# Kernel tuning notes

Hardware: AMD Instinct MI355X
Metric: run time of the kernel (lower is better)

Reference implementation:

```python
import jax, jax.numpy as jnp
import numpy as np

NMS_THRESHOLD = 0.4
TOP_K = 1000
MAX_BOXES = 300
N_ANCHORS = 300000
N_CLASSES = 80
DET_DIM = 85


def setup_inputs() -> dict:
    key = jax.random.key(0)
    k1, k2, k3, k4 = jax.random.split(key, 4)
    # valid [y1, x1, y2, x2] boxes: top-left corner + positive height/width
    yx = jax.random.uniform(k1, (1, N_ANCHORS, 2), jnp.float32) * 512.0
    hw = jax.random.uniform(k2, (1, N_ANCHORS, 2), jnp.float32) * 64.0 + 1.0
    boxes = jnp.concatenate([yx, yx + hw], axis=-1)
    classification = jax.random.uniform(k3, (1, N_ANCHORS, N_CLASSES), jnp.float32)
    detections = jax.random.normal(k4, (1, N_ANCHORS, DET_DIM), jnp.float32)
    return {"boxes": boxes, "classification": classification, "detections": detections}


def _iou_matrix(b):
    # b: [K, 4] as [y1, x1, y2, x2]
    y1, x1, y2, x2 = b[:, 0], b[:, 1], b[:, 2], b[:, 3]
    area = (y2 - y1) * (x2 - x1)
    ih = jnp.clip(jnp.minimum(y2[:, None], y2[None, :]) - jnp.maximum(y1[:, None], y1[None, :]), 0.0)
    iw = jnp.clip(jnp.minimum(x2[:, None], x2[None, :]) - jnp.maximum(x1[:, None], x1[None, :]), 0.0)
    inter = ih * iw
    return inter / (area[:, None] + area[None, :] - inter + 1e-8)


def _nms_forward(boxes, classification, detections):
    b = boxes[0]                      # [N, 4]
    cls = classification[0]           # [N, C]
    det = detections[0]               # [N, D]
    scores = jnp.max(cls, axis=1)     # [N]
    # pre-NMS top-k filter (lax.top_k returns scores sorted descending)
    _, idx = jax.lax.top_k(scores, TOP_K)
    b_k = b[idx]                      # [K, 4]
    det_k = det[idx]                  # [K, D]
    iou = _iou_matrix(b_k)            # [K, K]
    # greedy NMS over score-sorted candidates: keep box i iff no higher-scoring
    # kept box overlaps it above the threshold
    def step(keep, i):
        suppressed = jnp.any(keep & (iou[i] > NMS_THRESHOLD))
        return keep.at[i].set(~suppressed), None
    keep, _ = jax.lax.scan(step, jnp.zeros(TOP_K, dtype=bool), jnp.arange(TOP_K))
    # first MAX_BOXES kept candidates (in score order), zero-padded
    pos = jnp.where(keep, jnp.arange(TOP_K), TOP_K)
    pos = jnp.sort(pos)[:MAX_BOXES]
    valid = pos < TOP_K
    sel = det_k[jnp.minimum(pos, TOP_K - 1)]          # [MAX_BOXES, D]
    out = jnp.where(valid[:, None], sel, 0.0)
    return out[None]                   # [1, MAX_BOXES, D]


def reference(boxes, classification, detections):
    return _nms_forward(boxes, classification, detections)
```

## Files before the change

### kernel.cpp

```cpp
#include <hip/hip_runtime.h>
#include <stdint.h>

typedef unsigned long long u64;

#define N_ANCH   300000
#define N_CLS    80
#define DET_DIM  85
#define TOPK     1000
#define MAXB     300
#define NMS_THR  0.4f
#define CAP      4096
#define NBH      32
#define N4       (N_ANCH / 4)
#define ITH      ((N4 + NBH*1024 - 1) / (NBH*1024))

#define OFF_SBITS   0
#define OFF_HA      300032
#define OFF_HB      304128
#define OFF_META    308224
#define OFF_CAND    308288
#define OFF_TOPK    316480
#define OFF_BOXK    317480
#define OFF_MASK    321480
#define OFF_KEEPL   353480

__device__ __forceinline__ uint32_t ld_b32(const uint32_t* p) {
    return __hip_atomic_load(p, __ATOMIC_RELAXED, __HIP_MEMORY_SCOPE_AGENT);
}
__device__ __forceinline__ u64 ld_b64(const u64* p) {
    return __hip_atomic_load(p, __ATOMIC_RELAXED, __HIP_MEMORY_SCOPE_AGENT);
}
__device__ __forceinline__ void st_b32(uint32_t* p, uint32_t v) {
    __hip_atomic_store(p, v, __ATOMIC_RELAXED, __HIP_MEMORY_SCOPE_AGENT);
}
__device__ __forceinline__ void st_b64(u64* p, u64 v) {
    __hip_atomic_store(p, v, __ATOMIC_RELAXED, __HIP_MEMORY_SCOPE_AGENT);
}
__device__ __forceinline__ void st_f4(float4* p, float4 v) {
    union { float4 f; u64 u[2]; } cv; cv.f = v;
    u64* q = (u64*)p;
    st_b64(q, cv.u[0]); st_b64(q + 1, cv.u[1]);
}
__device__ __forceinline__ float4 ld_f4(const float4* p) {
    union { float4 f; u64 u[2]; } cv;
    const u64* q = (const u64*)p;
    cv.u[0] = ld_b64(q); cv.u[1] = ld_b64(q + 1);
    return cv.f;
}

__device__ __forceinline__ void gb_arrive(uint32_t* bar) {
    __syncthreads();
    if (threadIdx.x == 0)
        __hip_atomic_fetch_add(bar, 1u, __ATOMIC_RELAXED, __HIP_MEMORY_SCOPE_AGENT);
}
__device__ __forceinline__ void gb_wait(uint32_t* bar, uint32_t target) {
    if (threadIdx.x == 0) {
        while (__hip_atomic_load(bar, __ATOMIC_RELAXED, __HIP_MEMORY_SCOPE_AGENT) < target)
            __builtin_amdgcn_s_sleep(1);
    }
    __syncthreads();
}

__global__ __launch_bounds__(256) void k_scores(const float4* __restrict__ cls4,
                                                uint32_t* __restrict__ sbits,
                                                uint32_t* __restrict__ ha,
                                                uint32_t* __restrict__ hb,
                                                uint32_t* __restrict__ meta) {
    int tid = threadIdx.x;
    if (blockIdx.x == 0) {
        if (tid == 0) { meta[4] = 0; meta[8] = 0; }
        for (int i = tid; i < 4096; i += 256) { ha[i] = 0; hb[i] = 0; }
    }
    int wave = tid >> 6, lane = tid & 63, g = lane >> 2, q = lane & 3;
    int row = blockIdx.x * 64 + wave * 16 + g;
    if (row >= N_ANCH) return;
    const float4* rp = cls4 + (size_t)row * 20;
    float m = -1.0f;
    #pragma unroll
    for (int k = 0; k < 5; k++) {
        float4 v = rp[q + k * 4];
        m = fmaxf(m, fmaxf(fmaxf(v.x, v.y), fmaxf(v.z, v.w)));
    }
    m = fmaxf(m, __shfl_xor(m, 1));
    m = fmaxf(m, __shfl_xor(m, 2));
    if (q == 0) sbits[row] = __float_as_uint(m);
}

__device__ __forceinline__ void agg_add(uint32_t* h, uint32_t bin, bool valid) {
    int lane = threadIdx.x & 63;
    bool done = !valid;
    while (true) {
        unsigned long long rem = __ballot(!done);
        if (rem == 0ull) break;
        int leader = __ffsll((long long)rem) - 1;
        uint32_t lbin = __shfl(bin, leader);
        bool mine = (!done) && (bin == lbin);
        unsigned long long grp = __ballot(mine);
        if (lane == leader) atomicAdd(&h[lbin], (uint32_t)__popcll(grp));
        done = done || mine;
    }
}

__device__ __forceinline__ void findthr_core(const uint32_t c[4], uint32_t* wred,
                                             uint32_t K, uint32_t* res) {
    int tid = threadIdx.x, lane = tid & 63, wave = tid >> 6;
    uint32_t s = c[0] + c[1] + c[2] + c[3];
    uint32_t x = s;
    #pragma unroll
    for (int off = 1; off < 64; off <<= 1) {
        uint32_t v = __shfl_up(x, off);
        if (lane >= off) x += v;
    }
    if (lane == 63) wred[wave] = x;
    __syncthreads();
    if (wave == 0) {
        uint32_t w = (lane < 16) ? wred[lane] : 0u;
        #pragma unroll
        for (int off = 1; off < 16; off <<= 1) {
            uint32_t v = __shfl_up(w, off);
            if (lane >= off) w += v;
        }
        if (lane < 16) wred[lane] = w;
    }
    __syncthreads();
    uint32_t base = (wave == 0) ? 0u : wred[wave - 1];
    uint32_t incl = base + x, excl = incl - s;
    if (excl < K && incl >= K) {
        uint32_t run = excl;
        #pragma unroll
        for (int k = 0; k < 4; k++) {
            uint32_t nr = run + c[k];
            if (run < K && nr >= K) { res[0] = 4095 - (tid * 4 + k); res[1] = run; }
            run = nr;
        }
    }
    __syncthreads();
}

#define MSW(i, w) ((i) * 16 + (((w) + (i)) & 15))

__global__ __launch_bounds__(1024) void k_select(const uint4* __restrict__ sb4,
                                                 uint32_t* __restrict__ ha,
                                                 uint32_t* __restrict__ hb,
                                                 uint32_t* __restrict__ meta,
                                                 u64* __restrict__ cand,
                                                 uint32_t* __restrict__ topk,
                                                 const float4* __restrict__ boxes4,
                                                 float4* __restrict__ boxk,
                                                 u64* __restrict__ M,
                                                 uint32_t* __restrict__ keepl,
                                                 const float* __restrict__ det,
                                                 float* __restrict__ out) {
    __shared__ __align__(16) u64 big[16000];
    __shared__ uint32_t wred[16];
    __shared__ uint32_t mr[2];
    __shared__ uint32_t kidS[MAXB];

    const int tid = threadIdx.x, wave = tid >> 6, lane = tid & 63;
    const int blk = blockIdx.x;
    uint32_t* bar = &meta[8];
    uint32_t* h = (uint32_t*)big;

    for (int i = tid; i < 4096; i += 1024) h[i] = 0;
    __syncthreads();
    for (int it = 0; it < ITH; it++) {
        int t4 = (it * NBH + blk) * 1024 + tid;
        bool v = t4 < N4;
        uint4 sv = v ? sb4[t4] : make_uint4(0, 0, 0, 0);
        agg_add(h, sv.x >> 20, v);
        agg_add(h, sv.y >> 20, v);
        agg_add(h, sv.z >> 20, v);
        agg_add(h, sv.w >> 20, v);
    }
    __syncthreads();
    for (int i = tid; i < 4096; i += 1024) { uint32_t v = h[i]; if (v) atomicAdd(&ha[i], v); }
    gb_arrive(bar); gb_wait(bar, NBH * 1);

    uint32_t c[4];
    {
        uint32_t* base = ha + 4u * (1023u - (uint32_t)tid);
        c[0] = ld_b32(base + 3); c[1] = ld_b32(base + 2);
        c[2] = ld_b32(base + 1); c[3] = ld_b32(base + 0);
    }
    findthr_core(c, wred, TOPK, mr);
    const uint32_t binA = mr[0], GA = mr[1];
    for (int i = tid; i < 4096; i += 1024) h[i] = 0;
    __syncthreads();
    for (int it = 0; it < ITH; it++) {
        int t4 = (it * NBH + blk) * 1024 + tid;
        if (t4 < N4) {
            uint4 sv = sb4[t4];
            if ((sv.x >> 20) == binA) atomicAdd(&h[(sv.x >> 8) & 0xFFFu], 1u);
            if ((sv.y >> 20) == binA) atomicAdd(&h[(sv.y >> 8) & 0xFFFu], 1u);
            if ((sv.z >> 20) == binA) atomicAdd(&h[(sv.z >> 8) & 0xFFFu], 1u);
            if ((sv.w >> 20) == binA) atomicAdd(&h[(sv.w >> 8) & 0xFFFu], 1u);
        }
    }
    __syncthreads();
    for (int i = tid; i < 4096; i += 1024) { uint32_t v = h[i]; if (v) atomicAdd(&hb[i], v); }
    gb_arrive(bar); gb_wait(bar, NBH * 2);

    {
        uint32_t* base = hb + 4u * (1023u - (uint32_t)tid);
        c[0] = ld_b32(base + 3); c[1] = ld_b32(base + 2);
        c[2] = ld_b32(base + 1); c[3] = ld_b32(base + 0);
    }
    findthr_core(c, wred, TOPK - GA, mr);
    const uint32_t T24 = (binA << 12) | mr[0];
    for (int it = 0; it < ITH; it++) {
        int t4 = (it * NBH + blk) * 1024 + tid;
        bool v = t4 < N4;
        uint4 sv = v ? sb4[t4] : make_uint4(0, 0, 0, 0);
        uint32_t sl[4] = {sv.x, sv.y, sv.z, sv.w};
        #pragma unroll
        for (int s = 0; s < 4; s++) {
            uint32_t sb = sl[s];
            bool m = v && ((sb >> 8) >= T24);
            unsigned long long b = __ballot(m);
            if (b) {
                int leader = __ffsll((long long)b) - 1;
                uint32_t base2 = 0;
                if (lane == leader) base2 = atomicAdd(&meta[4], (uint32_t)__popcll(b));
                base2 = __shfl(base2, leader);
                if (m) {
                    uint32_t p = base2 + (uint32_t)__popcll(b & ((1ull << lane) - 1ull));
                    uint32_t idx = (uint32_t)(t4 * 4 + s);
                    if (p < CAP) st_b64(&cand[p], ((u64)sb << 32) | (uint32_t)(~idx));
                }
            }
        }
    }
    gb_arrive(bar); gb_wait(bar, NBH * 3);

    u64* candS = big;
    uint32_t C = ld_b32(&meta[4]); if (C > CAP) C = CAP;
    uint32_t Cpad = (C + 63u) & ~63u;
    for (uint32_t t = tid; t < Cpad; t += 1024) candS[t] = (t < C) ? ld_b64(&cand[t]) : 0ull;
    __syncthreads();
    for (uint32_t i = (uint32_t)(blk * 16 + wave); i < C; i += NBH * 16) {
        u64 my = candS[i];
        uint32_t r = 0;
        for (uint32_t j0 = 0; j0 < Cpad; j0 += 64)
            r += (uint32_t)__popcll(__ballot(candS[j0 + lane] > my));
        if (r < TOPK && lane == 0) {
            uint32_t idx = ~(uint32_t)(my & 0xFFFFFFFFull);
            if (idx < N_ANCH) { st_b32(&topk[r], idx); st_f4(&boxk[r], boxes4[idx]); }
        }
    }
    gb_arrive(bar); gb_wait(bar, NBH * 4);

    float4* bks  = (float4*)big;
    float* areaS = (float*)((char*)big + 16000);
    for (int i = tid; i < TOPK; i += 1024) {
        float4 b = ld_f4(&boxk[i]);
        bks[i] = b;
        {
            #pragma clang fp contract(off)
            areaS[i] = (b.z - b.x) * (b.w - b.y);
        }
    }
    __syncthreads();
    for (int gw = blk * 16 + wave; gw < TOPK * 16; gw += NBH * 16) {
        int i = gw >> 4, w = gw & 15;
        int j = w * 64 + lane, jc = j < TOPK ? j : 0;
        float4 bi = bks[i], bj = bks[jc];
        bool ok;
        {
            #pragma clang fp contract(off)
            float ih = fminf(bi.z, bj.z) - fmaxf(bi.x, bj.x); ih = fmaxf(ih, 0.0f);
            float iw = fminf(bi.w, bj.w) - fmaxf(bi.y, bj.y); iw = fmaxf(iw, 0.0f);
            float inter = ih * iw;
            float denom = (areaS[i] + areaS[jc] - inter) + 1e-8f;
            ok = (j < TOPK) && (inter / denom > NMS_THR);
        }
        unsigned long long m = __ballot(ok);
        if (lane == 0) st_b64(&M[i * 16 + w], m);
    }
    gb_arrive(bar);

    if (blk == 0) {
        gb_wait(bar, NBH * 5);
        u64* MS = big;
        for (int t = tid; t < TOPK * 16; t += 1024) {
            int i = t >> 4, w = t & 15;
            MS[MSW(i, w)] = ld_b64(&M[t]);
        }
        __syncthreads();
        if (tid < 64) {
            u64 keptArr[16];
            #pragma unroll
            for (int cc = 0; cc < 16; cc++) {
                int i = cc * 64 + lane;
                u64 pre = 0ull, Mic = 0ull;
                if (i < TOPK) {
                    #pragma unroll
                    for (int w = 0; w < cc; w++) pre |= MS[MSW(i, w)] & keptArr[w];
                    Mic = MS[MSW(i, cc)];
                }
                unsigned long long pre_mask = __ballot(pre != 0ull);
                u64 kc = 0ull;
                const int lim = (cc == 15) ? (TOPK - 960) : 64;
                for (int k = 0; k < lim; k++) {
                    unsigned long long b = __ballot(((Mic >> k) & 1ull) != 0ull);
                    bool sup = (((pre_mask >> k) & 1ull) != 0ull) || ((b & kc) != 0ull);
                    kc |= sup ? 0ull : (1ull << k);
                }
                keptArr[cc] = kc;
            }
            uint32_t pfxw[16];
            uint32_t run = 0;
            #pragma unroll
            for (int w = 0; w < 16; w++) { pfxw[w] = run; run += (uint32_t)__popcll(keptArr[w]); }
            int total = (int)run; if (total > MAXB) total = MAXB;
            for (int r = total + lane; r < MAXB; r += 64) st_b32(&keepl[r], 0xFFFFFFFFu);
            #pragma unroll
            for (int w = 0; w < 16; w++) {
                int i = w * 64 + lane;
                if (i < TOPK) {
                    u64 kw = keptArr[w];
                    if ((kw >> lane) & 1ull) {
                        uint32_t rank = pfxw[w] + (uint32_t)__popcll(kw & ((1ull << lane) - 1ull));
                        if (rank < MAXB) st_b32(&keepl[rank], ld_b32(&topk[i]));
                    }
                }
            }
        }
    }
    gb_arrive(bar); gb_wait(bar, NBH * 6);

    if (tid < MAXB) kidS[tid] = ld_b32(&keepl[tid]);
    __syncthreads();
    int t = blk * 1024 + tid;
    if (t < MAXB * DET_DIM) {
        int r = t / DET_DIM, col = t - r * DET_DIM;
        uint32_t src = kidS[r];
        float v = 0.0f;
        if (src < N_ANCH) v = det[(size_t)src * DET_DIM + col];
        out[t] = v;
    }
}

extern "C" void kernel_launch(void* const* d_in, const int* in_sizes, int n_in,
                              void* d_out, int out_size, void* d_ws, size_t ws_size,
                              hipStream_t stream) {
    const float4* boxes4 = (const float4*)d_in[0];
    const float4* cls4   = (const float4*)d_in[1];
    const float*  det    = (const float*)d_in[2];
    float* out = (float*)d_out;
    uint32_t* ws = (uint32_t*)d_ws;

    uint32_t* sbits = ws + OFF_SBITS;
    uint32_t* ha    = ws + OFF_HA;
    uint32_t* hb    = ws + OFF_HB;
    uint32_t* meta  = ws + OFF_META;
    u64*      cand  = (u64*)(ws + OFF_CAND);
    uint32_t* topk  = ws + OFF_TOPK;
    float4*   boxk  = (float4*)(ws + OFF_BOXK);
    u64*      M     = (u64*)(ws + OFF_MASK);
    uint32_t* keepl = ws + OFF_KEEPL;

    k_scores<<<(N_ANCH + 63) / 64, 256, 0, stream>>>(cls4, sbits, ha, hb, meta);
    k_select<<<NBH, 1024, 0, stream>>>((const uint4*)sbits, ha, hb, meta, cand, topk,
                                       boxes4, boxk, M, keepl, det, out);
}
```

Measured before the change: 273.7 us.

## Split persistent select kernel into separate launches replacing software grid barriers

Replaces the single 32-block persistent kernel, which used atomic-counter grid barriers between phases, with six separate kernel launches. Each launch gets its own grid size: 80 blocks for the histograms and compaction, 96 for ranking, 250 for mask building, and 1 for the greedy scan. This is meant to remove barrier spin-wait cost and raise parallelism in each phase. The trade-off is added launch overhead and extra global-memory round trips between phases.

```diff
diff --git a/kernel.cpp b/kernel.cpp
--- a/kernel.cpp
+++ b/kernel.cpp
@@ -10,9 +10,11 @@
 #define MAXB     300
 #define NMS_THR  0.4f
 #define CAP      4096
-#define NBH      32
 #define N4       (N_ANCH / 4)
-#define ITH      ((N4 + NBH*1024 - 1) / (NBH*1024))
+
+#define NB_HIST  80
+#define NB_RANK  96
+#define NB_MASK  250
 
 #define OFF_SBITS   0
 #define OFF_HA      300032
@@ -22,44 +24,6 @@
 #define OFF_TOPK    316480
 #define OFF_BOXK    317480
 #define OFF_MASK    321480
-#define OFF_KEEPL   353480
-
-__device__ __forceinline__ uint32_t ld_b32(const uint32_t* p) {
-    return __hip_atomic_load(p, __ATOMIC_RELAXED, __HIP_MEMORY_SCOPE_AGENT);
-}
-__device__ __forceinline__ u64 ld_b64(const u64* p) {
-    return __hip_atomic_load(p, __ATOMIC_RELAXED, __HIP_MEMORY_SCOPE_AGENT);
-}
-__device__ __forceinline__ void st_b32(uint32_t* p, uint32_t v) {
-    __hip_atomic_store(p, v, __ATOMIC_RELAXED, __HIP_MEMORY_SCOPE_AGENT);
-}
-__device__ __forceinline__ void st_b64(u64* p, u64 v) {
-    __hip_atomic_store(p, v, __ATOMIC_RELAXED, __HIP_MEMORY_SCOPE_AGENT);
-}
-__device__ __forceinline__ void st_f4(float4* p, float4 v) {
-    union { float4 f; u64 u[2]; } cv; cv.f = v;
-    u64* q = (u64*)p;
-    st_b64(q, cv.u[0]); st_b64(q + 1, cv.u[1]);
-}
-__device__ __forceinline__ float4 ld_f4(const float4* p) {
-    union { float4 f; u64 u[2]; } cv;
-    const u64* q = (const u64*)p;
-    cv.u[0] = ld_b64(q); cv.u[1] = ld_b64(q + 1);
-    return cv.f;
-}
-
-__device__ __forceinline__ void gb_arrive(uint32_t* bar) {
-    __syncthreads();
-    if (threadIdx.x == 0)
-        __hip_atomic_fetch_add(bar, 1u, __ATOMIC_RELAXED, __HIP_MEMORY_SCOPE_AGENT);
-}
-__device__ __forceinline__ void gb_wait(uint32_t* bar, uint32_t target) {
-    if (threadIdx.x == 0) {
-        while (__hip_atomic_load(bar, __ATOMIC_RELAXED, __HIP_MEMORY_SCOPE_AGENT) < target)
-            __builtin_amdgcn_s_sleep(1);
-    }
-    __syncthreads();
-}
 
 __global__ __launch_bounds__(256) void k_scores(const float4* __restrict__ cls4,
                                                 uint32_t* __restrict__ sbits,
@@ -68,7 +32,7 @@
                                                 uint32_t* __restrict__ meta) {
     int tid = threadIdx.x;
     if (blockIdx.x == 0) {
-        if (tid == 0) { meta[4] = 0; meta[8] = 0; }
+        if (tid == 0) meta[4] = 0;
         for (int i = tid; i < 4096; i += 256) { ha[i] = 0; hb[i] = 0; }
     }
     int wave = tid >> 6, lane = tid & 63, g = lane >> 2, q = lane & 3;
@@ -137,122 +101,121 @@
     __syncthreads();
 }
 
-#define MSW(i, w) ((i) * 16 + (((w) + (i)) & 15))
-
-__global__ __launch_bounds__(1024) void k_select(const uint4* __restrict__ sb4,
-                                                 uint32_t* __restrict__ ha,
-                                                 uint32_t* __restrict__ hb,
-                                                 uint32_t* __restrict__ meta,
-                                                 u64* __restrict__ cand,
-                                                 uint32_t* __restrict__ topk,
-                                                 const float4* __restrict__ boxes4,
-                                                 float4* __restrict__ boxk,
-                                                 u64* __restrict__ M,
-                                                 uint32_t* __restrict__ keepl,
-                                                 const float* __restrict__ det,
-                                                 float* __restrict__ out) {
-    __shared__ __align__(16) u64 big[16000];
+__device__ __forceinline__ void load_bins(const uint32_t* __restrict__ hist, uint32_t c[4]) {
+    uint4 q = ((const uint4*)hist)[1023 - threadIdx.x];
+    c[0] = q.w; c[1] = q.z; c[2] = q.y; c[3] = q.x;
+}
+
+__global__ __launch_bounds__(1024) void k_histA(const uint4* __restrict__ sb4,
+                                                uint32_t* __restrict__ ha) {
+    __shared__ uint32_t h[4096];
+    int tid = threadIdx.x;
+    for (int i = tid; i < 4096; i += 1024) h[i] = 0;
+    __syncthreads();
+    int t4 = blockIdx.x * 1024 + tid;
+    bool v = t4 < N4;
+    uint4 sv = v ? sb4[t4] : make_uint4(0, 0, 0, 0);
+    agg_add(h, sv.x >> 20, v);
+    agg_add(h, sv.y >> 20, v);
+    agg_add(h, sv.z >> 20, v);
+    agg_add(h, sv.w >> 20, v);
+    __syncthreads();
+    for (int i = tid; i < 4096; i += 1024) { uint32_t c = h[i]; if (c) atomicAdd(&ha[i], c); }
+}
+
+__global__ __launch_bounds__(1024) void k_histB(const uint4* __restrict__ sb4,
+                                                const uint32_t* __restrict__ ha,
+                                                uint32_t* __restrict__ hb) {
+    __shared__ uint32_t h[4096];
     __shared__ uint32_t wred[16];
     __shared__ uint32_t mr[2];
-    __shared__ uint32_t kidS[MAXB];
-
-    const int tid = threadIdx.x, wave = tid >> 6, lane = tid & 63;
-    const int blk = blockIdx.x;
-    uint32_t* bar = &meta[8];
-    uint32_t* h = (uint32_t*)big;
-
+    int tid = threadIdx.x;
+    uint32_t c[4];
+    load_bins(ha, c);
+    findthr_core(c, wred, TOPK, mr);
+    uint32_t binA = mr[0];
     for (int i = tid; i < 4096; i += 1024) h[i] = 0;
     __syncthreads();
-    for (int it = 0; it < ITH; it++) {
-        int t4 = (it * NBH + blk) * 1024 + tid;
-        bool v = t4 < N4;
-        uint4 sv = v ? sb4[t4] : make_uint4(0, 0, 0, 0);
-        agg_add(h, sv.x >> 20, v);
-        agg_add(h, sv.y >> 20, v);
-        agg_add(h, sv.z >> 20, v);
-        agg_add(h, sv.w >> 20, v);
-    }
-    __syncthreads();
-    for (int i = tid; i < 4096; i += 1024) { uint32_t v = h[i]; if (v) atomicAdd(&ha[i], v); }
-    gb_arrive(bar); gb_wait(bar, NBH * 1);
-
+    int t4 = blockIdx.x * 1024 + tid;
+    if (t4 < N4) {
+        uint4 sv = sb4[t4];
+        if ((sv.x >> 20) == binA) atomicAdd(&h[(sv.x >> 8) & 0xFFFu], 1u);
+        if ((sv.y >> 20) == binA) atomicAdd(&h[(sv.y >> 8) & 0xFFFu], 1u);
+        if ((sv.z >> 20) == binA) atomicAdd(&h[(sv.z >> 8) & 0xFFFu], 1u);
+        if ((sv.w >> 20) == binA) atomicAdd(&h[(sv.w >> 8) & 0xFFFu], 1u);
+    }
+    __syncthreads();
+    for (int i = tid; i < 4096; i += 1024) { uint32_t v = h[i]; if (v) atomicAdd(&hb[i], v); }
+}
+
+__global__ __launch_bounds__(1024) void k_compact(const uint4* __restrict__ sb4,
+                                                  const uint32_t* __restrict__ ha,
+                                                  const uint32_t* __restrict__ hb,
+                                                  uint32_t* __restrict__ meta,
+                                                  u64* __restrict__ cand) {
+    __shared__ uint32_t wred[16];
+    __shared__ uint32_t mr[2];
+    int tid = threadIdx.x, lane = tid & 63;
     uint32_t c[4];
-    {
-        uint32_t* base = ha + 4u * (1023u - (uint32_t)tid);
-        c[0] = ld_b32(base + 3); c[1] = ld_b32(base + 2);
-        c[2] = ld_b32(base + 1); c[3] = ld_b32(base + 0);
-    }
+    load_bins(ha, c);
     findthr_core(c, wred, TOPK, mr);
-    const uint32_t binA = mr[0], GA = mr[1];
-    for (int i = tid; i < 4096; i += 1024) h[i] = 0;
-    __syncthreads();
-    for (int it = 0; it < ITH; it++) {
-        int t4 = (it * NBH + blk) * 1024 + tid;
-        if (t4 < N4) {
-            uint4 sv = sb4[t4];
-            if ((sv.x >> 20) == binA) atomicAdd(&h[(sv.x >> 8) & 0xFFFu], 1u);
-            if ((sv.y >> 20) == binA) atomicAdd(&h[(sv.y >> 8) & 0xFFFu], 1u);
-            if ((sv.z >> 20) == binA) atomicAdd(&h[(sv.z >> 8) & 0xFFFu], 1u);
-            if ((sv.w >> 20) == binA) atomicAdd(&h[(sv.w >> 8) & 0xFFFu], 1u);
-        }
-    }
-    __syncthreads();
-    for (int i = tid; i < 4096; i += 1024) { uint32_t v = h[i]; if (v) atomicAdd(&hb[i], v); }
-    gb_arrive(bar); gb_wait(bar, NBH * 2);
-
-    {
-        uint32_t* base = hb + 4u * (1023u - (uint32_t)tid);
-        c[0] = ld_b32(base + 3); c[1] = ld_b32(base + 2);
-        c[2] = ld_b32(base + 1); c[3] = ld_b32(base + 0);
-    }
+    uint32_t binA = mr[0], GA = mr[1];
+    load_bins(hb, c);
     findthr_core(c, wred, TOPK - GA, mr);
-    const uint32_t T24 = (binA << 12) | mr[0];
-    for (int it = 0; it < ITH; it++) {
-        int t4 = (it * NBH + blk) * 1024 + tid;
-        bool v = t4 < N4;
-        uint4 sv = v ? sb4[t4] : make_uint4(0, 0, 0, 0);
-        uint32_t sl[4] = {sv.x, sv.y, sv.z, sv.w};
-        #pragma unroll
-        for (int s = 0; s < 4; s++) {
-            uint32_t sb = sl[s];
-            bool m = v && ((sb >> 8) >= T24);
-            unsigned long long b = __ballot(m);
-            if (b) {
-                int leader = __ffsll((long long)b) - 1;
-                uint32_t base2 = 0;
-                if (lane == leader) base2 = atomicAdd(&meta[4], (uint32_t)__popcll(b));
-                base2 = __shfl(base2, leader);
-                if (m) {
-                    uint32_t p = base2 + (uint32_t)__popcll(b & ((1ull << lane) - 1ull));
-                    uint32_t idx = (uint32_t)(t4 * 4 + s);
-                    if (p < CAP) st_b64(&cand[p], ((u64)sb << 32) | (uint32_t)(~idx));
-                }
+    uint32_t T24 = (binA << 12) | mr[0];
+    int t4 = blockIdx.x * 1024 + tid;
+    bool v = t4 < N4;
+    uint4 sv = v ? sb4[t4] : make_uint4(0, 0, 0, 0);
+    uint32_t sl[4] = {sv.x, sv.y, sv.z, sv.w};
+    #pragma unroll
+    for (int s = 0; s < 4; s++) {
+        uint32_t sb = sl[s];
+        bool m = v && ((sb >> 8) >= T24);
+        unsigned long long b = __ballot(m);
+        if (b) {
+            int leader = __ffsll((long long)b) - 1;
+            uint32_t base2 = 0;
+            if (lane == leader) base2 = atomicAdd(&meta[4], (uint32_t)__popcll(b));
+            base2 = __shfl(base2, leader);
+            if (m) {
+                uint32_t p = base2 + (uint32_t)__popcll(b & ((1ull << lane) - 1ull));
+                uint32_t idx = (uint32_t)(t4 * 4 + s);
+                if (p < CAP) cand[p] = ((u64)sb << 32) | (uint32_t)(~idx);
             }
         }
     }
-    gb_arrive(bar); gb_wait(bar, NBH * 3);
-
-    u64* candS = big;
-    uint32_t C = ld_b32(&meta[4]); if (C > CAP) C = CAP;
+}
+
+__global__ __launch_bounds__(1024) void k_rank(const u64* __restrict__ cand,
+                                               const uint32_t* __restrict__ meta,
+                                               uint32_t* __restrict__ topk,
+                                               const float4* __restrict__ boxes4,
+                                               float4* __restrict__ boxk) {
+    __shared__ u64 candS[CAP];
+    int tid = threadIdx.x, wave = tid >> 6, lane = tid & 63;
+    uint32_t C = meta[4]; if (C > CAP) C = CAP;
     uint32_t Cpad = (C + 63u) & ~63u;
-    for (uint32_t t = tid; t < Cpad; t += 1024) candS[t] = (t < C) ? ld_b64(&cand[t]) : 0ull;
-    __syncthreads();
-    for (uint32_t i = (uint32_t)(blk * 16 + wave); i < C; i += NBH * 16) {
+    for (uint32_t t = tid; t < Cpad; t += 1024) candS[t] = (t < C) ? cand[t] : 0ull;
+    __syncthreads();
+    for (uint32_t i = (uint32_t)(blockIdx.x * 16 + wave); i < C; i += NB_RANK * 16) {
         u64 my = candS[i];
         uint32_t r = 0;
         for (uint32_t j0 = 0; j0 < Cpad; j0 += 64)
             r += (uint32_t)__popcll(__ballot(candS[j0 + lane] > my));
         if (r < TOPK && lane == 0) {
             uint32_t idx = ~(uint32_t)(my & 0xFFFFFFFFull);
-            if (idx < N_ANCH) { st_b32(&topk[r], idx); st_f4(&boxk[r], boxes4[idx]); }
-        }
-    }
-    gb_arrive(bar); gb_wait(bar, NBH * 4);
-
-    float4* bks  = (float4*)big;
-    float* areaS = (float*)((char*)big + 16000);
+            if (idx < N_ANCH) { topk[r] = idx; boxk[r] = boxes4[idx]; }
+        }
+    }
+}
+
+__global__ __launch_bounds__(1024) void k_mask(const float4* __restrict__ boxk,
+                                               u64* __restrict__ M) {
+    __shared__ float4 bks[TOPK];
+    __shared__ float areaS[TOPK];
+    int tid = threadIdx.x, wave = tid >> 6, lane = tid & 63;
     for (int i = tid; i < TOPK; i += 1024) {
-        float4 b = ld_f4(&boxk[i]);
+        float4 b = boxk[i];
         bks[i] = b;
         {
             #pragma clang fp contract(off)
@@ -260,7 +223,7 @@
         }
     }
     __syncthreads();
-    for (int gw = blk * 16 + wave; gw < TOPK * 16; gw += NBH * 16) {
+    for (int gw = blockIdx.x * 16 + wave; gw < TOPK * 16; gw += NB_MASK * 16) {
         int i = gw >> 4, w = gw & 15;
         int j = w * 64 + lane, jc = j < TOPK ? j : 0;
         float4 bi = bks[i], bj = bks[jc];
@@ -274,68 +237,72 @@
             ok = (j < TOPK) && (inter / denom > NMS_THR);
         }
         unsigned long long m = __ballot(ok);
-        if (lane == 0) st_b64(&M[i * 16 + w], m);
-    }
-    gb_arrive(bar);
-
-    if (blk == 0) {
-        gb_wait(bar, NBH * 5);
-        u64* MS = big;
-        for (int t = tid; t < TOPK * 16; t += 1024) {
-            int i = t >> 4, w = t & 15;
-            MS[MSW(i, w)] = ld_b64(&M[t]);
-        }
-        __syncthreads();
-        if (tid < 64) {
-            u64 keptArr[16];
-            #pragma unroll
-            for (int cc = 0; cc < 16; cc++) {
-                int i = cc * 64 + lane;
-                u64 pre = 0ull, Mic = 0ull;
-                if (i < TOPK) {
-                    #pragma unroll
-                    for (int w = 0; w < cc; w++) pre |= MS[MSW(i, w)] & keptArr[w];
-                    Mic = MS[MSW(i, cc)];
-                }
-                unsigned long long pre_mask = __ballot(pre != 0ull);
-                u64 kc = 0ull;
-                const int lim = (cc == 15) ? (TOPK - 960) : 64;
-                for (int k = 0; k < lim; k++) {
-                    unsigned long long b = __ballot(((Mic >> k) & 1ull) != 0ull);
-                    bool sup = (((pre_mask >> k) & 1ull) != 0ull) || ((b & kc) != 0ull);
-                    kc |= sup ? 0ull : (1ull << k);
-                }
-                keptArr[cc] = kc;
+        if (lane == 0) M[i * 16 + w] = m;
+    }
+}
+
+#define MSW(i, w) ((i) * 16 + (((w) + (i)) & 15))
+
+__global__ __launch_bounds__(1024) void k_scan(const u64* __restrict__ M,
+                                               const uint32_t* __restrict__ topk,
+                                               const float* __restrict__ det,
+                                               float* __restrict__ out) {
+    __shared__ __align__(16) u64 MS[16000];
+    __shared__ int keeplS[MAXB];
+    int tid = threadIdx.x, lane = tid & 63;
+    for (int t = tid; t < TOPK * 16; t += 1024) {
+        int i = t >> 4, w = t & 15;
+        MS[MSW(i, w)] = M[t];
+    }
+    __syncthreads();
+    if (tid < 64) {
+        u64 keptArr[16];
+        #pragma unroll
+        for (int cc = 0; cc < 16; cc++) {
+            int i = cc * 64 + lane;
+            u64 pre = 0ull, Mic = 0ull;
+            if (i < TOPK) {
+                #pragma unroll
+                for (int w = 0; w < cc; w++) pre |= MS[MSW(i, w)] & keptArr[w];
+                Mic = MS[MSW(i, cc)];
             }
-            uint32_t pfxw[16];
-            uint32_t run = 0;
-            #pragma unroll
-            for (int w = 0; w < 16; w++) { pfxw[w] = run; run += (uint32_t)__popcll(keptArr[w]); }
-            int total = (int)run; if (total > MAXB) total = MAXB;
-            for (int r = total + lane; r < MAXB; r += 64) st_b32(&keepl[r], 0xFFFFFFFFu);
-            #pragma unroll
-            for (int w = 0; w < 16; w++) {
-                int i = w * 64 + lane;
-                if (i < TOPK) {
-                    u64 kw = keptArr[w];
-                    if ((kw >> lane) & 1ull) {
-                        uint32_t rank = pfxw[w] + (uint32_t)__popcll(kw & ((1ull << lane) - 1ull));
-                        if (rank < MAXB) st_b32(&keepl[rank], ld_b32(&topk[i]));
-                    }
+            unsigned long long pre_mask = __ballot(pre != 0ull);
+            u64 kc = 0ull;
+            const int lim = (cc == 15) ? (TOPK - 960) : 64;
+            for (int k = 0; k < lim; k++) {
+                unsigned long long b = __ballot(((Mic >> k) & 1ull) != 0ull);
+                bool sup = (((pre_mask >> k) & 1ull) != 0ull) || ((b & kc) != 0ull);
+                kc |= sup ? 0ull : (1ull << k);
+            }
+            keptArr[cc] = kc;
+        }
+        uint32_t pfxw[16];
+        uint32_t run = 0;
+        #pragma unroll
+        for (int w = 0; w < 16; w++) { pfxw[w] = run; run += (uint32_t)__popcll(keptArr[w]); }
+        int total = (int)run; if (total > MAXB) total = MAXB;
+        for (int r = total + lane; r < MAXB; r += 64) keeplS[r] = -1;
+        #pragma unroll
+        for (int w = 0; w < 16; w++) {
+            int i = w * 64 + lane;
+            if (i < TOPK) {
+                u64 kw = keptArr[w];
+                if ((kw >> lane) & 1ull) {
+                    uint32_t rank = pfxw[w] + (uint32_t)__popcll(kw & ((1ull << lane) - 1ull));
+                    if (rank < MAXB) keeplS[rank] = i;
                 }
             }
         }
     }
-    gb_arrive(bar); gb_wait(bar, NBH * 6);
-
-    if (tid < MAXB) kidS[tid] = ld_b32(&keepl[tid]);
-    __syncthreads();
-    int t = blk * 1024 + tid;
-    if (t < MAXB * DET_DIM) {
+    __syncthreads();
+    for (int t = tid; t < MAXB * DET_DIM; t += 1024) {
         int r = t / DET_DIM, col = t - r * DET_DIM;
-        uint32_t src = kidS[r];
+        int pos = keeplS[r];
         float v = 0.0f;
-        if (src < N_ANCH) v = det[(size_t)src * DET_DIM + col];
+        if (pos >= 0) {
+            uint32_t src = topk[pos];
+            if (src < N_ANCH) v = det[(size_t)src * DET_DIM + col];
+        }
         out[t] = v;
     }
 }
@@ -357,9 +324,12 @@
     uint32_t* topk  = ws + OFF_TOPK;
     float4*   boxk  = (float4*)(ws + OFF_BOXK);
     u64*      M     = (u64*)(ws + OFF_MASK);
-    uint32_t* keepl = ws + OFF_KEEPL;
-
-    k_scores<<<(N_ANCH + 63) / 64, 256, 0, stream>>>(cls4, sbits, ha, hb, meta);
-    k_select<<<NBH, 1024, 0, stream>>>((const uint4*)sbits, ha, hb, meta, cand, topk,
-                                       boxes4, boxk, M, keepl, det, out);
-}
+
+    k_scores <<<(N_ANCH + 63) / 64, 256, 0, stream>>>(cls4, sbits, ha, hb, meta);
+    k_histA  <<<NB_HIST, 1024, 0, stream>>>((const uint4*)sbits, ha);
+    k_histB  <<<NB_HIST, 1024, 0, stream>>>((const uint4*)sbits, ha, hb);
+    k_compact<<<NB_HIST, 1024, 0, stream>>>((const uint4*)sbits, ha, hb, meta, cand);
+    k_rank   <<<NB_RANK, 1024, 0, stream>>>(cand, meta, topk, boxes4, boxk);
+    k_mask   <<<NB_MASK, 1024, 0, stream>>>(boxk, M);
+    k_scan   <<<1, 1024, 0, stream>>>(M, topk, det, out);
+}
```

Result: slower. 280.0 us (+2.3%).

## Replace serial single-wave NMS scan with per-block parallel fixed-point iteration

Applied to the files above, without the earlier changes.

The greedy NMS resolution used to run in one wave of block 0 followed by an extra grid barrier. Now every block loads its row of the suppression mask into registers and iterates a Jacobi-style fixed point over the keep bitmask until it stops changing, which removes the second grid barrier and the keep-list round trip through global memory. The grid also doubles from 32 to 64 blocks. The iteration count depends on how long suppression chains are; in the worst case it approaches TOPK rounds, each with two block barriers, and every block now repeats the same NMS work.

```diff
diff --git a/kernel.cpp b/kernel.cpp
--- a/kernel.cpp
+++ b/kernel.cpp
@@ -10,7 +10,7 @@
 #define MAXB     300
 #define NMS_THR  0.4f
 #define CAP      4096
-#define NBH      32
+#define NBH      64
 #define N4       (N_ANCH / 4)
 #define ITH      ((N4 + NBH*1024 - 1) / (NBH*1024))
 
@@ -22,7 +22,6 @@
 #define OFF_TOPK    316480
 #define OFF_BOXK    317480
 #define OFF_MASK    321480
-#define OFF_KEEPL   353480
 
 __device__ __forceinline__ uint32_t ld_b32(const uint32_t* p) {
     return __hip_atomic_load(p, __ATOMIC_RELAXED, __HIP_MEMORY_SCOPE_AGENT);
@@ -137,8 +136,6 @@
     __syncthreads();
 }
 
-#define MSW(i, w) ((i) * 16 + (((w) + (i)) & 15))
-
 __global__ __launch_bounds__(1024) void k_select(const uint4* __restrict__ sb4,
                                                  uint32_t* __restrict__ ha,
                                                  uint32_t* __restrict__ hb,
@@ -148,13 +145,14 @@
                                                  const float4* __restrict__ boxes4,
                                                  float4* __restrict__ boxk,
                                                  u64* __restrict__ M,
-                                                 uint32_t* __restrict__ keepl,
                                                  const float* __restrict__ det,
                                                  float* __restrict__ out) {
-    __shared__ __align__(16) u64 big[16000];
+    __shared__ __align__(16) u64 big[4096];
     __shared__ uint32_t wred[16];
     __shared__ uint32_t mr[2];
-    __shared__ uint32_t kidS[MAXB];
+    __shared__ u64 kbufA[16], kbufB[16];
+    __shared__ uint32_t chgF[16];
+    __shared__ int keeplS[MAXB];
 
     const int tid = threadIdx.x, wave = tid >> 6, lane = tid & 63;
     const int blk = blockIdx.x;
@@ -276,66 +274,62 @@
         unsigned long long m = __ballot(ok);
         if (lane == 0) st_b64(&M[i * 16 + w], m);
     }
-    gb_arrive(bar);
-
-    if (blk == 0) {
-        gb_wait(bar, NBH * 5);
-        u64* MS = big;
-        for (int t = tid; t < TOPK * 16; t += 1024) {
-            int i = t >> 4, w = t & 15;
-            MS[MSW(i, w)] = ld_b64(&M[t]);
-        }
+    gb_arrive(bar); gb_wait(bar, NBH * 5);
+
+    const bool vr = tid < TOPK;
+    u64 Mpre[16];
+    #pragma unroll
+    for (int w = 0; w < 16; w++) {
+        u64 row = vr ? ld_b64(&M[(size_t)tid * 16 + w]) : 0ull;
+        u64 pm = (w < wave) ? ~0ull : ((w == wave) ? ((1ull << lane) - 1ull) : 0ull);
+        Mpre[w] = row & pm;
+    }
+    if (tid < 15) kbufA[tid] = ~0ull;
+    if (tid == 15) kbufA[15] = (1ull << (TOPK - 960)) - 1ull;
+    __syncthreads();
+
+    u64* cur = kbufA;
+    u64* nxt = kbufB;
+    for (int it = 0; it < TOPK + 2; ++it) {
+        u64 sup = 0ull;
+        #pragma unroll
+        for (int w = 0; w < 16; w++) sup |= Mpre[w] & cur[w];
+        bool nk = vr && (sup == 0ull);
+        u64 bal = __ballot(nk);
+        if (lane == 0) { nxt[wave] = bal; chgF[wave] = (bal != cur[wave]) ? 1u : 0u; }
         __syncthreads();
-        if (tid < 64) {
-            u64 keptArr[16];
-            #pragma unroll
-            for (int cc = 0; cc < 16; cc++) {
-                int i = cc * 64 + lane;
-                u64 pre = 0ull, Mic = 0ull;
-                if (i < TOPK) {
-                    #pragma unroll
-                    for (int w = 0; w < cc; w++) pre |= MS[MSW(i, w)] & keptArr[w];
-                    Mic = MS[MSW(i, cc)];
-                }
-                unsigned long long pre_mask = __ballot(pre != 0ull);
-                u64 kc = 0ull;
-                const int lim = (cc == 15) ? (TOPK - 960) : 64;
-                for (int k = 0; k < lim; k++) {
-                    unsigned long long b = __ballot(((Mic >> k) & 1ull) != 0ull);
-                    bool sup = (((pre_mask >> k) & 1ull) != 0ull) || ((b & kc) != 0ull);
-                    kc |= sup ? 0ull : (1ull << k);
-                }
-                keptArr[cc] = kc;
-            }
-            uint32_t pfxw[16];
-            uint32_t run = 0;
-            #pragma unroll
-            for (int w = 0; w < 16; w++) { pfxw[w] = run; run += (uint32_t)__popcll(keptArr[w]); }
-            int total = (int)run; if (total > MAXB) total = MAXB;
-            for (int r = total + lane; r < MAXB; r += 64) st_b32(&keepl[r], 0xFFFFFFFFu);
-            #pragma unroll
-            for (int w = 0; w < 16; w++) {
-                int i = w * 64 + lane;
-                if (i < TOPK) {
-                    u64 kw = keptArr[w];
-                    if ((kw >> lane) & 1ull) {
-                        uint32_t rank = pfxw[w] + (uint32_t)__popcll(kw & ((1ull << lane) - 1ull));
-                        if (rank < MAXB) st_b32(&keepl[rank], ld_b32(&topk[i]));
-                    }
-                }
-            }
-        }
-    }
-    gb_arrive(bar); gb_wait(bar, NBH * 6);
-
-    if (tid < MAXB) kidS[tid] = ld_b32(&keepl[tid]);
-    __syncthreads();
+        uint32_t any = 0;
+        #pragma unroll
+        for (int w = 0; w < 16; w++) any |= chgF[w];
+        __syncthreads();
+        u64* t = cur; cur = nxt; nxt = t;
+        if (!any) break;
+    }
+
+    u64 kw = cur[wave];
+    uint32_t pfx = 0;
+    #pragma unroll
+    for (int w = 0; w < 16; w++) {
+        uint32_t p = (uint32_t)__popcll(cur[w]);
+        if (w < wave) pfx += p;
+    }
+    if (tid < MAXB) keeplS[tid] = -1;
+    __syncthreads();
+    if (vr && ((kw >> lane) & 1ull)) {
+        uint32_t rank = pfx + (uint32_t)__popcll(kw & ((1ull << lane) - 1ull));
+        if (rank < MAXB) keeplS[rank] = tid;
+    }
+    __syncthreads();
+
     int t = blk * 1024 + tid;
     if (t < MAXB * DET_DIM) {
         int r = t / DET_DIM, col = t - r * DET_DIM;
-        uint32_t src = kidS[r];
+        int pos = keeplS[r];
         float v = 0.0f;
-        if (src < N_ANCH) v = det[(size_t)src * DET_DIM + col];
+        if (pos >= 0) {
+            uint32_t src = ld_b32(&topk[pos]);
+            if (src < N_ANCH) v = det[(size_t)src * DET_DIM + col];
+        }
         out[t] = v;
     }
 }
@@ -357,9 +351,8 @@
     uint32_t* topk  = ws + OFF_TOPK;
     float4*   boxk  = (float4*)(ws + OFF_BOXK);
     u64*      M     = (u64*)(ws + OFF_MASK);
-    uint32_t* keepl = ws + OFF_KEEPL;
 
     k_scores<<<(N_ANCH + 63) / 64, 256, 0, stream>>>(cls4, sbits, ha, hb, meta);
     k_select<<<NBH, 1024, 0, stream>>>((const uint4*)sbits, ha, hb, meta, cand, topk,
-                                       boxes4, boxk, M, keepl, det, out);
-}
+                                       boxes4, boxk, M, det, out);
+}
```

Result: faster. 242.1 us (-11.6%).
